# Optimization experiments

Measured on AMD Instinct MI355X. Metric: run time of the kernel, lower is better.

Reference implementation:

```python
import jax, jax.numpy as jnp
import numpy as np

D_MODEL = 1024
HEAD = 16
HEAD_DIM = D_MODEL // HEAD


def setup_inputs() -> dict:
    key = jax.random.key(0)
    ks = jax.random.split(key, 11)
    B, S = 2, 2048
    q = jax.random.normal(ks[0], (B, S, D_MODEL), dtype=jnp.float32)
    k = jax.random.normal(ks[1], (B, S, D_MODEL), dtype=jnp.float32)
    v = jax.random.normal(ks[2], (B, S, D_MODEL), dtype=jnp.float32)
    # nn.Linear-style params: weight [out, in], bias [out]
    w_scale = 1.0 / np.sqrt(D_MODEL)
    def lin(kk):
        kw, kb = jax.random.split(kk)
        W = jax.random.uniform(kw, (D_MODEL, D_MODEL), jnp.float32, -w_scale, w_scale)
        b = jax.random.uniform(kb, (D_MODEL,), jnp.float32, -w_scale, w_scale)
        return W, b
    Wq, bq = lin(ks[3])
    Wk, bk = lin(ks[4])
    Wv, bv = lin(ks[5])
    Wo, bo = lin(ks[6])
    return {"query": q, "key": k, "value": v,
            "Wq": Wq, "bq": bq, "Wk": Wk, "bk": bk,
            "Wv": Wv, "bv": bv, "Wo": Wo, "bo": bo}


def reference(query, key, value, Wq, bq, Wk, bk, Wv, bv, Wo, bo):
    B, S, _ = query.shape
    # QKV projections (nn.Linear: x @ W.T + b)
    q = query @ Wq.T + bq
    k = key @ Wk.T + bk
    v = value @ Wv.T + bv
    # b s (h d) -> b h s d
    def split_heads(t):
        return t.reshape(B, -1, HEAD, HEAD_DIM).transpose(0, 2, 1, 3)
    q, k, v = split_heads(q), split_heads(k), split_heads(v)
    # NOTE: original forward never applies self.scale, and its masked_fill is
    # non-inplace (result discarded), so scores are raw QK^T with no masking.
    scores = jnp.einsum('bhid,bhjd->bhij', q, k)
    attn = jax.nn.softmax(scores, axis=-1)
    out = jnp.einsum('bhij,bhjd->bhid', attn, v)
    # b h s d -> b s (h d)
    out = out.transpose(0, 2, 1, 3).reshape(B, S, D_MODEL)
    # output projection (dropout=0.0)
    return out @ Wo.T + bo
```

## Files before the change

kernel.cpp:

```cpp
#include <hip/hip_runtime.h>
#include <stdint.h>

#define DM   1024
#define SEQ  2048
#define NH   16
#define HD   64
#define SHIFT 14.0f

typedef _Float16 f16;
typedef f16   half8 __attribute__((ext_vector_type(8)));
typedef f16   half4 __attribute__((ext_vector_type(4)));
typedef float f32x4 __attribute__((ext_vector_type(4)));
typedef float f32x16 __attribute__((ext_vector_type(16)));
typedef unsigned int u32;
typedef u32 u32x4 __attribute__((ext_vector_type(4)));

__device__ __forceinline__ void gl_lds16(const void* g, void* l) {
  __builtin_amdgcn_global_load_lds(
      reinterpret_cast<__attribute__((address_space(1))) u32*>(reinterpret_cast<uintptr_t>(g)),
      reinterpret_cast<__attribute__((address_space(3))) u32*>(reinterpret_cast<uintptr_t>(l)),
      16, 0, 0);
}

__device__ __forceinline__ u32 pkrtz(float a, float b) {
  auto h = __builtin_amdgcn_cvt_pkrtz(a, b);
  return __builtin_bit_cast(u32, h);
}

__global__ __launch_bounds__(256) void cast_all(
    const float* __restrict__ q, const float* __restrict__ k, const float* __restrict__ v,
    const float* __restrict__ Wq, const float* __restrict__ Wk,
    const float* __restrict__ Wv, const float* __restrict__ Wo,
    f16* __restrict__ qh, f16* __restrict__ kh, f16* __restrict__ vh,
    f16* __restrict__ Wqh, f16* __restrict__ Wkh, f16* __restrict__ Wvh,
    f16* __restrict__ Woh) {
  int i = blockIdx.x * 256 + threadIdx.x;
  const float* s;
  f16* d;
  int off;
  float sc = 1.0f;
  if (i < 1572864) {
    int sel = i >> 19;
    off = i & 524287;
    s = sel == 0 ? q : sel == 1 ? k : v;
    d = sel == 0 ? qh : sel == 1 ? kh : vh;
  } else {
    int j = i - 1572864;
    int sel = j >> 17;
    off = j & 131071;
    s = sel == 0 ? Wq : sel == 1 ? Wk : sel == 2 ? Wv : Wo;
    d = sel == 0 ? Wqh : sel == 1 ? Wkh : sel == 2 ? Wvh : Woh;
    if (sel == 0) sc = 1.44269504f;
  }
  const float4* s4 = reinterpret_cast<const float4*>(s);
  float4 a = s4[2 * (size_t)off];
  float4 b = s4[2 * (size_t)off + 1];
  half8 o;
  o[0] = (f16)(sc * a.x); o[1] = (f16)(sc * a.y); o[2] = (f16)(sc * a.z); o[3] = (f16)(sc * a.w);
  o[4] = (f16)(sc * b.x); o[5] = (f16)(sc * b.y); o[6] = (f16)(sc * b.z); o[7] = (f16)(sc * b.w);
  *reinterpret_cast<half8*>(d + 8 * (size_t)off) = o;
}

#define GEMM_BODY(ATYPE, LOADA)                                                \
  __shared__ f16 As[2][128 * 64];                                              \
  __shared__ f16 Ws[2][128 * 64];                                              \
  int t = threadIdx.x;                                                         \
  int w = t >> 6, lane = t & 63, lr = lane & 15, lk = lane >> 4;               \
  int m0 = blockIdx.y * 128, n0 = blockIdx.x * 128;                            \
  int wr = (w >> 1) * 64, wc = (w & 1) * 64;                                   \
  int rloc = 8 * w + (lane >> 3);                                   \
  int swc = (lane & 7) ^ (lane >> 3);               \
  const ATYPE* ga = A + (size_t)(m0 + rloc) * DM + swc * 8;                    \
  const f16* gw = W + (size_t)(n0 + rloc) * DM + swc * 8;                      \
  f32x4 zero4 = {0.f, 0.f, 0.f, 0.f};                                          \
  f32x4 acc[4][4];                                                             \
  _Pragma("unroll") for (int mb = 0; mb < 4; ++mb)                             \
      _Pragma("unroll") for (int nb = 0; nb < 4; ++nb) acc[mb][nb] = zero4;    \
  _Pragma("unroll") for (int j = 0; j < 4; ++j) {                              \
    LOADA(ga + (size_t)(32 * j) * DM, &As[0][j * 2048 + t * 8]);               \
    gl_lds16(gw + (size_t)(32 * j) * DM, &Ws[0][j * 2048 + t * 8]);            \
  }                                                                            \
  __syncthreads();                                                             \
  for (int kt = 0; kt < DM / 64; ++kt) {                                       \
    int cur = kt & 1;                                                          \
    if (kt + 1 < DM / 64) {                                                    \
      int k0 = (kt + 1) * 64;                                                  \
      _Pragma("unroll") for (int j = 0; j < 4; ++j) {                          \
        LOADA(ga + (size_t)(32 * j) * DM + k0, &As[cur ^ 1][j * 2048 + t * 8]);\
        gl_lds16(gw + (size_t)(32 * j) * DM + k0, &Ws[cur ^ 1][j * 2048 + t * 8]);\
      }                                                                        \
    }                                                                          \
    _Pragma("unroll") for (int ks = 0; ks < 2; ++ks) {                         \
      half8 af[4], wf[4];                                                      \
      _Pragma("unroll") for (int mb = 0; mb < 4; ++mb) {                       \
        int R = wr + mb * 16 + lr;                                             \
        int c = (ks * 64 + lk * 16) ^ ((lr & 7) << 4);                         \
        af[mb] = *reinterpret_cast<const half8*>(                              \
            reinterpret_cast<const char*>(&As[cur][0]) + R * 128 + c);         \
      }                                                                        \
      _Pragma("unroll") for (int nb = 0; nb < 4; ++nb) {                       \
        int R = wc + nb * 16 + lr;                                             \
        int c = (ks * 64 + lk * 16) ^ ((lr & 7) << 4);                         \
        wf[nb] = *reinterpret_cast<const half8*>(                              \
            reinterpret_cast<const char*>(&Ws[cur][0]) + R * 128 + c);         \
      }                                                                        \
      _Pragma("unroll") for (int mb = 0; mb < 4; ++mb)                         \
          _Pragma("unroll") for (int nb = 0; nb < 4; ++nb)                     \
              acc[mb][nb] = __builtin_amdgcn_mfma_f32_16x16x32_f16(            \
                  af[mb], wf[nb], acc[mb][nb], 0, 0, 0);                       \
    }                                                                          \
    __syncthreads();                                                           \
  }

__global__ __launch_bounds__(256) void gemm_qkv(
    const f16* __restrict__ A0, const f16* __restrict__ A1, const f16* __restrict__ A2,
    const f16* __restrict__ W0, const f16* __restrict__ W1, const f16* __restrict__ W2,
    const float* __restrict__ b0, const float* __restrict__ b1, const float* __restrict__ b2,
    f16* __restrict__ C0, f16* __restrict__ C1, f16* __restrict__ C2) {
  int z = blockIdx.z;
  const f16* A = (z == 0) ? A0 : (z == 1) ? A1 : A2;
  const f16* W = (z == 0) ? W0 : (z == 1) ? W1 : W2;
  const float* bias = (z == 0) ? b0 : (z == 1) ? b1 : b2;

  GEMM_BODY(f16, gl_lds16)

  float bscale = (z == 0) ? 1.44269504f : 1.0f;
  float bv[4];
#pragma unroll
  for (int nb = 0; nb < 4; ++nb) bv[nb] = bias[n0 + wc + nb * 16 + lr] * bscale;

  int lk4 = (lane >> 4) * 4;
  if (z == 2) {
#pragma unroll
    for (int mb = 0; mb < 4; ++mb)
#pragma unroll
      for (int nb = 0; nb < 4; ++nb) {
        int r0 = m0 + wr + mb * 16 + lk4;
        int c = n0 + wc + nb * 16 + lr;
        int b_ = r0 >> 11, s_ = r0 & 2047;
        int h_ = c >> 6, d_ = c & 63;
        f16* dst = C2 + (((size_t)(b_ * NH + h_) * HD + d_) * SEQ + s_);
        half4 hv;
#pragma unroll
        for (int j = 0; j < 4; ++j) hv[j] = (f16)(acc[mb][nb][j] + bv[nb]);
        *reinterpret_cast<half4*>(dst) = hv;
      }
  } else {
    f16* C = (z == 0) ? C0 : C1;
#pragma unroll
    for (int mb = 0; mb < 4; ++mb)
#pragma unroll
      for (int nb = 0; nb < 4; ++nb)
#pragma unroll
        for (int j = 0; j < 4; ++j) {
          int r = m0 + wr + mb * 16 + lk4 + j;
          int c = n0 + wc + nb * 16 + lr;
          C[(size_t)r * DM + c] = (f16)(acc[mb][nb][j] + bv[nb]);
        }
  }
}

__global__ __launch_bounds__(256) void gemm_out(
    const f16* __restrict__ A, const f16* __restrict__ W,
    const float* __restrict__ bias, float* __restrict__ C) {
  GEMM_BODY(f16, gl_lds16)

  float bv[4];
#pragma unroll
  for (int nb = 0; nb < 4; ++nb) bv[nb] = bias[n0 + wc + nb * 16 + lr];
  int lk4 = (lane >> 4) * 4;
#pragma unroll
  for (int mb = 0; mb < 4; ++mb)
#pragma unroll
    for (int nb = 0; nb < 4; ++nb)
#pragma unroll
      for (int j = 0; j < 4; ++j) {
        int r = m0 + wr + mb * 16 + lk4 + j;
        int c = n0 + wc + nb * 16 + lr;
        C[(size_t)r * DM + c] = acc[mb][nb][j] + bv[nb];
      }
}

__global__ __launch_bounds__(256) void attn_fwd15(const f16* __restrict__ Qg,
                                                  const f16* __restrict__ Kg,
                                                  const f16* __restrict__ VTg,
                                                  f16* __restrict__ Og) {
  int bid = blockIdx.x;
  int xcd = bid & 7;
  int slot = bid >> 3;
  int qt = slot & 15;
  int gh = slot >> 4;
  int bh = xcd | (gh << 3);
  int b = bh >> 4, h = bh & 15;

  size_t baseq = (size_t)b * SEQ * DM + (size_t)h * HD;
  const f16* Kp = Kg + baseq;
  const f16* VTp = VTg + (size_t)bh * HD * SEQ;

  __shared__ f16 Kl[2][64 * 128];
  __shared__ f16 Vl[2][64 * 128];

  int t = threadIdx.x;
  int w = t >> 6, lane = t & 63;
  int l31 = lane & 31, lh = lane >> 5;
  int vrow = t >> 4, vcb = t & 15;

  int tt = t >> 4;
  int ku = t & 15;
  int ke = (2 * tt) & 15;
  int kx = ku ^ ke;
  int ksel = (kx >> 3) & 1;
  int kcc = ksel ? ((kx ^ 1) & 7) : kx;
  int kvbase = 2 * tt + ksel;
  const f16* gK = Kp + (size_t)kvbase * DM + kcc * 8;
  const f16* gV = VTp + (size_t)vrow * SEQ + (vcb ^ vrow) * 8;
  f16* lK = &Kl[0][t * 8];
  f16* lV = &Vl[0][vrow * 128 + vcb * 8];
  const int KSTEP = 128 * DM;
  const int VSTEP = 128;
  const int LBK = 64 * 128;
  const int LBV = 64 * 128;

  int qs = qt * 128 + w * 32 + l31;
  const f16* Qrow = Qg + baseq + (size_t)qs * DM;
  half8 qf[4];
#pragma unroll
  for (int s = 0; s < 4; ++s)
    qf[s] = *reinterpret_cast<const half8*>(Qrow + s * 16 + lh * 8);

  auto stage = [&](int kt, int buf) {
    int ko = kt * KSTEP, vo = kt * VSTEP;
#pragma unroll
    for (int j = 0; j < 4; ++j)
      gl_lds16(gK + ko + (size_t)(32 * j) * DM, lK + buf * LBK + j * 2048);
#pragma unroll
    for (int j = 0; j < 4; ++j)
      gl_lds16(gV + vo + (size_t)(16 * j) * SEQ, lV + buf * LBV + j * 16 * 128);
  };
  auto readKf = [&](int buf, int nbk, int s) -> half8 {
    int kv = nbk * 32 + l31;
    int cc = s * 2 + lh;
    int u = (((kv & 1) << 3) | cc) ^ (kv & 15);
    return *reinterpret_cast<const half8*>(
        reinterpret_cast<const char*>(&Kl[buf][0]) + (kv >> 1) * 256 + (u << 4));
  };
  auto readVf = [&](int buf, int mb, int ks) -> half8 {
    int d = mb * 32 + l31;
    int c = (ks * 32 + lh * 16) ^ ((d & 15) << 4);
    return *reinterpret_cast<const half8*>(
        reinterpret_cast<const char*>(&Vl[buf][0]) + d * 256 + c);
  };

  f32x16 mShift, o0, o1;
#pragma unroll
  for (int i = 0; i < 16; ++i) {
    mShift[i] = -SHIFT;
    o0[i] = 0.f;
    o1[i] = 0.f;
  }
  float l_r = 0.f;

  stage(0, 0);
  __syncthreads();

  const int NT = SEQ / 128;
  for (int kt = 0; kt < NT; ++kt) {
    int cur = kt & 1;
    if (kt + 1 < NT) stage(kt + 1, cur ^ 1);

    __builtin_amdgcn_s_setprio(1);
    half8 k0 = readKf(cur, 0, 0);
    half8 k1 = readKf(cur, 1, 0);
    half8 k2 = readKf(cur, 2, 0);
    half8 k3 = readKf(cur, 3, 0);
    f32x16 s0 = __builtin_amdgcn_mfma_f32_32x32x16_f16(k0, qf[0], mShift, 0, 0, 0);
    f32x16 s1 = __builtin_amdgcn_mfma_f32_32x32x16_f16(k1, qf[0], mShift, 0, 0, 0);
    f32x16 s2 = __builtin_amdgcn_mfma_f32_32x32x16_f16(k2, qf[0], mShift, 0, 0, 0);
    f32x16 s3 = __builtin_amdgcn_mfma_f32_32x32x16_f16(k3, qf[0], mShift, 0, 0, 0);
#pragma unroll
    for (int s = 1; s < 4; ++s) {
      k0 = readKf(cur, 0, s);
      k1 = readKf(cur, 1, s);
      k2 = readKf(cur, 2, s);
      k3 = readKf(cur, 3, s);
      s0 = __builtin_amdgcn_mfma_f32_32x32x16_f16(k0, qf[s], s0, 0, 0, 0);
      s1 = __builtin_amdgcn_mfma_f32_32x32x16_f16(k1, qf[s], s1, 0, 0, 0);
      s2 = __builtin_amdgcn_mfma_f32_32x32x16_f16(k2, qf[s], s2, 0, 0, 0);
      s3 = __builtin_amdgcn_mfma_f32_32x32x16_f16(k3, qf[s], s3, 0, 0, 0);
    }
    __builtin_amdgcn_s_setprio(0);

    float rs0 = 0.f, rs1 = 0.f, rs2 = 0.f, rs3 = 0.f;
#pragma unroll
    for (int i = 0; i < 16; ++i) { s0[i] = __builtin_amdgcn_exp2f(s0[i]); rs0 += s0[i]; }
#pragma unroll
    for (int i = 0; i < 16; ++i) { s1[i] = __builtin_amdgcn_exp2f(s1[i]); rs1 += s1[i]; }
#pragma unroll
    for (int i = 0; i < 16; ++i) { s2[i] = __builtin_amdgcn_exp2f(s2[i]); rs2 += s2[i]; }
#pragma unroll
    for (int i = 0; i < 16; ++i) { s3[i] = __builtin_amdgcn_exp2f(s3[i]); rs3 += s3[i]; }
    l_r += (rs0 + rs1) + (rs2 + rs3);

#define PVSTEP(SP, NBK)                                                        \
    {                                                                          \
      u32 u0 = pkrtz(SP[0], SP[1]);                                            \
      u32 u1 = pkrtz(SP[2], SP[3]);                                            \
      u32 u2 = pkrtz(SP[4], SP[5]);                                            \
      u32 u3 = pkrtz(SP[6], SP[7]);                                            \
      u32 u4 = pkrtz(SP[8], SP[9]);                                            \
      u32 u5 = pkrtz(SP[10], SP[11]);                                          \
      u32 u6 = pkrtz(SP[12], SP[13]);                                          \
      u32 u7 = pkrtz(SP[14], SP[15]);                                          \
      asm volatile("v_permlane32_swap_b32 %0, %1" : "+v"(u0), "+v"(u2));       \
      asm volatile("v_permlane32_swap_b32 %0, %1" : "+v"(u1), "+v"(u3));       \
      asm volatile("v_permlane32_swap_b32 %0, %1" : "+v"(u4), "+v"(u6));       \
      asm volatile("v_permlane32_swap_b32 %0, %1" : "+v"(u5), "+v"(u7));       \
      u32x4 w0 = {u0, u1, u2, u3};                                             \
      u32x4 w1 = {u4, u5, u6, u7};                                             \
      half8 pa0 = __builtin_bit_cast(half8, w0);                               \
      half8 pa1 = __builtin_bit_cast(half8, w1);                               \
      half8 va = readVf(cur, 0, 2 * NBK);                                      \
      half8 vb = readVf(cur, 1, 2 * NBK);                                      \
      __builtin_amdgcn_s_setprio(1);                                           \
      o0 = __builtin_amdgcn_mfma_f32_32x32x16_f16(va, pa0, o0, 0, 0, 0);       \
      o1 = __builtin_amdgcn_mfma_f32_32x32x16_f16(vb, pa0, o1, 0, 0, 0);       \
      __builtin_amdgcn_s_setprio(0);                                           \
      va = readVf(cur, 0, 2 * NBK + 1);                                        \
      vb = readVf(cur, 1, 2 * NBK + 1);                                        \
      __builtin_amdgcn_s_setprio(1);                                           \
      o0 = __builtin_amdgcn_mfma_f32_32x32x16_f16(va, pa1, o0, 0, 0, 0);       \
      o1 = __builtin_amdgcn_mfma_f32_32x32x16_f16(vb, pa1, o1, 0, 0, 0);       \
      __builtin_amdgcn_s_setprio(0);                                           \
    }
    PVSTEP(s0, 0)
    PVSTEP(s1, 1)
    PVSTEP(s2, 2)
    PVSTEP(s3, 3)
#undef PVSTEP

    __syncthreads();
  }

  float l_all = l_r + __shfl_xor(l_r, 32);
  float inv = 1.0f / l_all;
  f16* Orow = Og + baseq + (size_t)qs * DM;
#pragma unroll
  for (int mb = 0; mb < 2; ++mb) {
    const f32x16& oo = mb ? o1 : o0;
#pragma unroll
    for (int rq = 0; rq < 4; ++rq) {
      half4 hv;
      hv[0] = (f16)(oo[4 * rq + 0] * inv);
      hv[1] = (f16)(oo[4 * rq + 1] * inv);
      hv[2] = (f16)(oo[4 * rq + 2] * inv);
      hv[3] = (f16)(oo[4 * rq + 3] * inv);
      *reinterpret_cast<half4*>(Orow + mb * 32 + 8 * rq + 4 * lh) = hv;
    }
  }
}

extern "C" void kernel_launch(void* const* d_in, const int* in_sizes, int n_in,
                              void* d_out, int out_size, void* d_ws, size_t ws_size,
                              hipStream_t stream) {
  (void)in_sizes; (void)n_in; (void)out_size; (void)ws_size;
  const float* q  = (const float*)d_in[0];
  const float* k  = (const float*)d_in[1];
  const float* v  = (const float*)d_in[2];
  const float* Wq = (const float*)d_in[3];
  const float* bq = (const float*)d_in[4];
  const float* Wk = (const float*)d_in[5];
  const float* bk = (const float*)d_in[6];
  const float* Wv = (const float*)d_in[7];
  const float* bv = (const float*)d_in[8];
  const float* Wo = (const float*)d_in[9];
  const float* bo = (const float*)d_in[10];
  float* out = (float*)d_out;

  char* ws = (char*)d_ws;
  const size_t MB = 1u << 20;
  f16* qh  = (f16*)(ws + 0 * MB);
  f16* kh  = (f16*)(ws + 8 * MB);
  f16* vh  = (f16*)(ws + 16 * MB);
  f16* Wqh = (f16*)(ws + 24 * MB);
  f16* Wkh = (f16*)(ws + 26 * MB);
  f16* Wvh = (f16*)(ws + 28 * MB);
  f16* Woh = (f16*)(ws + 30 * MB);
  f16* Qp  = (f16*)(ws + 32 * MB);
  f16* Kp  = (f16*)(ws + 40 * MB);
  f16* Vtp = (f16*)(ws + 48 * MB);
  f16* At  = (f16*)(ws + 56 * MB);

  cast_all<<<8192, 256, 0, stream>>>(q, k, v, Wq, Wk, Wv, Wo,
                                     qh, kh, vh, Wqh, Wkh, Wvh, Woh);
  gemm_qkv<<<dim3(8, 32, 3), 256, 0, stream>>>(qh, kh, vh, Wqh, Wkh, Wvh,
                                               bq, bk, bv, Qp, Kp, Vtp);
  attn_fwd15<<<512, 256, 0, stream>>>(Qp, Kp, Vtp, At);
  gemm_out<<<dim3(8, 32), 256, 0, stream>>>(At, Woh, bo, out);
}
```

Before: 127.1 us.

## Halve GEMM N-tile to 64 and remap blocks XCD-aware for more parallelism

```diff
diff --git a/kernel.cpp b/kernel.cpp
--- a/kernel.cpp
+++ b/kernel.cpp
@@ -61,56 +61,62 @@
   *reinterpret_cast<half8*>(d + 8 * (size_t)off) = o;
 }
 
-#define GEMM_BODY(ATYPE, LOADA)                                                \
+#define GEMM_BODY_N64                                                          \
   __shared__ f16 As[2][128 * 64];                                              \
-  __shared__ f16 Ws[2][128 * 64];                                              \
+  __shared__ f16 Ws[2][64 * 64];                                               \
   int t = threadIdx.x;                                                         \
   int w = t >> 6, lane = t & 63, lr = lane & 15, lk = lane >> 4;               \
-  int m0 = blockIdx.y * 128, n0 = blockIdx.x * 128;                            \
-  int wr = (w >> 1) * 64, wc = (w & 1) * 64;                                   \
-  int rloc = 8 * w + (lane >> 3);                                   \
-  int swc = (lane & 7) ^ (lane >> 3);               \
-  const ATYPE* ga = A + (size_t)(m0 + rloc) * DM + swc * 8;                    \
+  int wr = (w >> 1) * 64, wc = (w & 1) * 32;                                   \
+  int rloc = 8 * w + (lane >> 3);                                              \
+  int swc = (lane & 7) ^ (lane >> 3);                                          \
+  const f16* ga = A + (size_t)(m0 + rloc) * DM + swc * 8;                      \
   const f16* gw = W + (size_t)(n0 + rloc) * DM + swc * 8;                      \
   f32x4 zero4 = {0.f, 0.f, 0.f, 0.f};                                          \
-  f32x4 acc[4][4];                                                             \
+  f32x4 acc[4][2];                                                             \
   _Pragma("unroll") for (int mb = 0; mb < 4; ++mb)                             \
-      _Pragma("unroll") for (int nb = 0; nb < 4; ++nb) acc[mb][nb] = zero4;    \
-  _Pragma("unroll") for (int j = 0; j < 4; ++j) {                              \
-    LOADA(ga + (size_t)(32 * j) * DM, &As[0][j * 2048 + t * 8]);               \
+      _Pragma("unroll") for (int nb = 0; nb < 2; ++nb) acc[mb][nb] = zero4;    \
+  _Pragma("unroll") for (int j = 0; j < 4; ++j)                                \
+    gl_lds16(ga + (size_t)(32 * j) * DM, &As[0][j * 2048 + t * 8]);            \
+  _Pragma("unroll") for (int j = 0; j < 2; ++j)                                \
     gl_lds16(gw + (size_t)(32 * j) * DM, &Ws[0][j * 2048 + t * 8]);            \
-  }                                                                            \
   __syncthreads();                                                             \
   for (int kt = 0; kt < DM / 64; ++kt) {                                       \
     int cur = kt & 1;                                                          \
     if (kt + 1 < DM / 64) {                                                    \
       int k0 = (kt + 1) * 64;                                                  \
-      _Pragma("unroll") for (int j = 0; j < 4; ++j) {                          \
-        LOADA(ga + (size_t)(32 * j) * DM + k0, &As[cur ^ 1][j * 2048 + t * 8]);\
+      _Pragma("unroll") for (int j = 0; j < 4; ++j)                            \
+        gl_lds16(ga + (size_t)(32 * j) * DM + k0, &As[cur ^ 1][j * 2048 + t * 8]);\
+      _Pragma("unroll") for (int j = 0; j < 2; ++j)                            \
         gl_lds16(gw + (size_t)(32 * j) * DM + k0, &Ws[cur ^ 1][j * 2048 + t * 8]);\
-      }                                                                        \
     }                                                                          \
     _Pragma("unroll") for (int ks = 0; ks < 2; ++ks) {                         \
-      half8 af[4], wf[4];                                                      \
+      half8 af[4], wf[2];                                                      \
       _Pragma("unroll") for (int mb = 0; mb < 4; ++mb) {                       \
         int R = wr + mb * 16 + lr;                                             \
         int c = (ks * 64 + lk * 16) ^ ((lr & 7) << 4);                         \
         af[mb] = *reinterpret_cast<const half8*>(                              \
             reinterpret_cast<const char*>(&As[cur][0]) + R * 128 + c);         \
       }                                                                        \
-      _Pragma("unroll") for (int nb = 0; nb < 4; ++nb) {                       \
+      _Pragma("unroll") for (int nb = 0; nb < 2; ++nb) {                       \
         int R = wc + nb * 16 + lr;                                             \
         int c = (ks * 64 + lk * 16) ^ ((lr & 7) << 4);                         \
         wf[nb] = *reinterpret_cast<const half8*>(                              \
             reinterpret_cast<const char*>(&Ws[cur][0]) + R * 128 + c);         \
       }                                                                        \
       _Pragma("unroll") for (int mb = 0; mb < 4; ++mb)                         \
-          _Pragma("unroll") for (int nb = 0; nb < 4; ++nb)                     \
+          _Pragma("unroll") for (int nb = 0; nb < 2; ++nb)                     \
               acc[mb][nb] = __builtin_amdgcn_mfma_f32_16x16x32_f16(            \
                   af[mb], wf[nb], acc[mb][nb], 0, 0, 0);                       \
     }                                                                          \
     __syncthreads();                                                           \
   }
+
+#define XCD_DECODE_N64                                                         \
+  int bid = blockIdx.x;                                                        \
+  int xcd = bid & 7;                                                           \
+  int idx = bid >> 3;                                               \
+  int m0 = (xcd * 4 + (idx >> 4)) * 128;                                       \
+  int n0 = (idx & 15) * 64;
 
 __global__ __launch_bounds__(256) void gemm_qkv(
     const f16* __restrict__ A0, const f16* __restrict__ A1, const f16* __restrict__ A2,
@@ -122,19 +128,20 @@
   const f16* W = (z == 0) ? W0 : (z == 1) ? W1 : W2;
   const float* bias = (z == 0) ? b0 : (z == 1) ? b1 : b2;
 
-  GEMM_BODY(f16, gl_lds16)
+  XCD_DECODE_N64
+  GEMM_BODY_N64
 
   float bscale = (z == 0) ? 1.44269504f : 1.0f;
-  float bv[4];
-#pragma unroll
-  for (int nb = 0; nb < 4; ++nb) bv[nb] = bias[n0 + wc + nb * 16 + lr] * bscale;
-
-  int lk4 = (lane >> 4) * 4;
+  float bv[2];
+#pragma unroll
+  for (int nb = 0; nb < 2; ++nb) bv[nb] = bias[n0 + wc + nb * 16 + lr] * bscale;
+
+  int lk4 = lk * 4;
   if (z == 2) {
 #pragma unroll
     for (int mb = 0; mb < 4; ++mb)
 #pragma unroll
-      for (int nb = 0; nb < 4; ++nb) {
+      for (int nb = 0; nb < 2; ++nb) {
         int r0 = m0 + wr + mb * 16 + lk4;
         int c = n0 + wc + nb * 16 + lr;
         int b_ = r0 >> 11, s_ = r0 & 2047;
@@ -150,7 +157,7 @@
 #pragma unroll
     for (int mb = 0; mb < 4; ++mb)
 #pragma unroll
-      for (int nb = 0; nb < 4; ++nb)
+      for (int nb = 0; nb < 2; ++nb)
 #pragma unroll
         for (int j = 0; j < 4; ++j) {
           int r = m0 + wr + mb * 16 + lk4 + j;
@@ -163,16 +170,17 @@
 __global__ __launch_bounds__(256) void gemm_out(
     const f16* __restrict__ A, const f16* __restrict__ W,
     const float* __restrict__ bias, float* __restrict__ C) {
-  GEMM_BODY(f16, gl_lds16)
-
-  float bv[4];
-#pragma unroll
-  for (int nb = 0; nb < 4; ++nb) bv[nb] = bias[n0 + wc + nb * 16 + lr];
-  int lk4 = (lane >> 4) * 4;
+  XCD_DECODE_N64
+  GEMM_BODY_N64
+
+  float bv[2];
+#pragma unroll
+  for (int nb = 0; nb < 2; ++nb) bv[nb] = bias[n0 + wc + nb * 16 + lr];
+  int lk4 = lk * 4;
 #pragma unroll
   for (int mb = 0; mb < 4; ++mb)
 #pragma unroll
-    for (int nb = 0; nb < 4; ++nb)
+    for (int nb = 0; nb < 2; ++nb)
 #pragma unroll
       for (int j = 0; j < 4; ++j) {
         int r = m0 + wr + mb * 16 + lk4 + j;
@@ -392,8 +400,8 @@
 
   cast_all<<<8192, 256, 0, stream>>>(q, k, v, Wq, Wk, Wv, Wo,
                                      qh, kh, vh, Wqh, Wkh, Wvh, Woh);
-  gemm_qkv<<<dim3(8, 32, 3), 256, 0, stream>>>(qh, kh, vh, Wqh, Wkh, Wvh,
-                                               bq, bk, bv, Qp, Kp, Vtp);
+  gemm_qkv<<<dim3(512, 1, 3), 256, 0, stream>>>(qh, kh, vh, Wqh, Wkh, Wvh,
+                                                bq, bk, bv, Qp, Kp, Vtp);
   attn_fwd15<<<512, 256, 0, stream>>>(Qp, Kp, Vtp, At);
-  gemm_out<<<dim3(8, 32), 256, 0, stream>>>(At, Woh, bo, out);
-}
+  gemm_out<<<512, 256, 0, stream>>>(At, Woh, bo, out);
+}
```

Result: faster. 113.2 us (-10.9%).
